# Performance work log

Hardware: AMD Instinct MI355X
Metric: run time of the kernel (lower is better)

Reference implementation:

```python
import jax, jax.numpy as jnp
import numpy as np

HEADS = 8


def setup_inputs() -> dict:
    key = jax.random.key(0)
    ks = jax.random.split(key, 7)
    B, C, H, W = 8, 512, 64, 64
    K, MEM = 64, 512
    s = 0.02
    return {
        "x": jax.random.normal(ks[0], (B, C, H, W), dtype=jnp.float32),
        "Ft": jax.random.normal(ks[1], (B, K, MEM), dtype=jnp.float32),
        "Wq": jax.random.normal(ks[2], (C, C), dtype=jnp.float32) * s,
        "Wk": jax.random.normal(ks[3], (C, MEM), dtype=jnp.float32) * s,
        "Wv": jax.random.normal(ks[4], (C, MEM), dtype=jnp.float32) * s,
        "Wp": jax.random.normal(ks[5], (C, C), dtype=jnp.float32) * s,
        "bp": jax.random.normal(ks[6], (C,), dtype=jnp.float32) * s,
    }


def reference(x, Ft, Wq, Wk, Wv, Wp, bp):
    B, C, H, W = x.shape
    h = HEADS
    d = C // h
    N = H * W
    # 1x1 conv query projection: (out_c, in_c) applied over spatial dims
    q = jnp.einsum('oc,bchw->bohw', Wq, x).reshape(B, h, d, N)
    q = jnp.transpose(q, (0, 1, 3, 2))                      # [B,h,N,d]
    # Linear K/V on memory tokens: Ft [B,K,MEM] @ W^T -> [B,K,C]
    k = (Ft @ Wk.T).reshape(B, -1, h, d).transpose(0, 2, 1, 3)  # [B,h,K,d]
    v = (Ft @ Wv.T).reshape(B, -1, h, d).transpose(0, 2, 1, 3)  # [B,h,K,d]
    attn = jnp.einsum('bhnc,bhkc->bhnk', q, k) / jnp.sqrt(jnp.float32(d))
    attn = jax.nn.softmax(attn, axis=-1)
    out = jnp.einsum('bhnk,bhkc->bhnc', attn, v)            # [B,h,N,d]
    out = jnp.transpose(out, (0, 1, 3, 2)).reshape(B, C, H, W)
    out = jnp.einsum('oc,bchw->bohw', Wp, out) + bp[None, :, None, None]
    return x + out
```

## Files before the change

### kernel.cpp

```cpp
#include <hip/hip_runtime.h>
#include <cstdint>
#include <cstddef>

#define BATCH 8
#define CDIM  512
#define NPIX  4096
#define NHEAD 8
#define DH    64
#define KTOK  64
#define MEM   512

#define SSTR 40
#define QSTR 72

typedef __attribute__((ext_vector_type(8))) short          bf8;
typedef __attribute__((ext_vector_type(4))) float          f4;
typedef __attribute__((ext_vector_type(4))) unsigned short us4;

__device__ __forceinline__ unsigned short f2bf(float f){
  union { float f; unsigned int u; } x; x.f = f;
  unsigned int r = (x.u + 0x7fffu + ((x.u >> 16) & 1u)) >> 16;
  return (unsigned short)r;
}

__global__ __launch_bounds__(256) void wconv(const float* __restrict__ wq, const float* __restrict__ wp,
                                             unsigned short* __restrict__ wqb, unsigned short* __restrict__ wpb){
  int i = (blockIdx.x * 256 + threadIdx.x) * 4;
  float4 a = *(const float4*)(wq + i);
  us4 pa = { f2bf(a.x), f2bf(a.y), f2bf(a.z), f2bf(a.w) };
  *(us4*)(wqb + i) = pa;
  float4 b = *(const float4*)(wp + i);
  us4 pb = { f2bf(b.x), f2bf(b.y), f2bf(b.z), f2bf(b.w) };
  *(us4*)(wpb + i) = pb;
}

__global__ __launch_bounds__(256) void xtrans(const float* __restrict__ x, unsigned short* __restrict__ xb){
  __shared__ __align__(16) unsigned short t[64 * 68];
  int tid = threadIdx.x;
  int n0 = blockIdx.x * 64, c0 = blockIdx.y * 64, b = blockIdx.z;
  const float* xp = x + ((size_t)(b * CDIM + c0)) * NPIX + n0;
#pragma unroll
  for (int it = 0; it < 4; ++it){
    int idx = it * 1024 + tid * 4;
    int cc = idx >> 6, nn = idx & 63;
    float4 v = *(const float4*)(xp + (size_t)cc * NPIX + nn);
    us4 pk = { f2bf(v.x), f2bf(v.y), f2bf(v.z), f2bf(v.w) };
    *(us4*)&t[cc * 68 + nn] = pk;
  }
  __syncthreads();
  unsigned short* op = xb + ((size_t)(b * NPIX + n0)) * CDIM + c0;
#pragma unroll
  for (int it = 0; it < 4; ++it){
    int idx = it * 1024 + tid * 4;
    int nn = idx >> 6, c4 = idx & 63;
    us4 pk = { t[(c4 + 0) * 68 + nn], t[(c4 + 1) * 68 + nn],
               t[(c4 + 2) * 68 + nn], t[(c4 + 3) * 68 + nn] };
    *(us4*)(op + (size_t)nn * CDIM + c4) = pk;
  }
}

__global__ __launch_bounds__(256) void kvproj(const float* __restrict__ Ft, const float* __restrict__ Wk,
                                              const float* __restrict__ Wv, unsigned short* __restrict__ kb,
                                              unsigned short* __restrict__ vt){
  __shared__ float ft[8][MEM];
  int tid = threadIdx.x;
  int cg = blockIdx.x, kk0 = blockIdx.y * 8, b = blockIdx.z;
  const float* fp = Ft + ((size_t)(b * KTOK + kk0)) * MEM;
#pragma unroll
  for (int it = 0; it < 4; ++it){
    int idx = it * 1024 + tid * 4;
    int row = idx >> 9, m = idx & 511;
    *(float4*)&ft[row][m] = *(const float4*)(fp + (size_t)row * MEM + m);
  }
  __syncthreads();
  int kv = tid >> 7, cl = tid & 127;
  int c = cg * 128 + cl;
  const float* wrow = (kv ? Wv : Wk) + (size_t)c * MEM;
  float acc[8] = {0.f,0.f,0.f,0.f,0.f,0.f,0.f,0.f};
  for (int m = 0; m < MEM; m += 4){
    float4 wv4 = *(const float4*)(wrow + m);
#pragma unroll
    for (int kk = 0; kk < 8; ++kk){
      acc[kk] += wv4.x * ft[kk][m] + wv4.y * ft[kk][m+1] + wv4.z * ft[kk][m+2] + wv4.w * ft[kk][m+3];
    }
  }
  int h = c >> 6, dd = c & 63;
  if (kv == 0){
#pragma unroll
    for (int kk = 0; kk < 8; ++kk)
      kb[(((size_t)(b * NHEAD + h)) * KTOK + kk0 + kk) * DH + dd] = f2bf(acc[kk] * 0.125f);
  } else {
#pragma unroll
    for (int kk = 0; kk < 8; ++kk)
      vt[(((size_t)(b * NHEAD + h)) * DH + dd) * KTOK + kk0 + kk] = f2bf(acc[kk]);
  }
}

__global__ __launch_bounds__(256, 2) void qattn(const unsigned short* __restrict__ wqb,
                                                const unsigned short* __restrict__ xb,
                                                const unsigned short* __restrict__ kb,
                                                const unsigned short* __restrict__ vt,
                                                unsigned short* __restrict__ att){
  __shared__ __align__(16) unsigned short ab[4 * 64 * QSTR];
  __shared__ __align__(16) unsigned short pbuf[4 * 64 * QSTR];
  int tid = threadIdx.x;
  int w = tid >> 6, l = tid & 63;
  int lo = l & 15, hi = l >> 4;
  int n0 = blockIdx.x * 128, o0 = blockIdx.y * 128, b = blockIdx.z;
  int ol = (w >> 1) * 64, nl = (w & 1) * 64;

  f4 z = {0.f, 0.f, 0.f, 0.f};
  f4 accq[4][4];
#pragma unroll
  for (int i = 0; i < 4; ++i)
#pragma unroll
    for (int j = 0; j < 4; ++j) accq[i][j] = z;

  int srow = tid >> 2;
  int scol = (tid & 3) * 8;
  const unsigned short* ap = wqb + ((size_t)(o0 + srow)) * CDIM + scol;
  const unsigned short* bp = xb + ((size_t)(b * NPIX + n0 + srow)) * CDIM + scol;
  unsigned short* as0 = &ab[srow * SSTR + scol];
  unsigned short* as1 = &ab[(srow + 64) * SSTR + scol];
  unsigned short* bs0 = &ab[5120 + srow * SSTR + scol];
  unsigned short* bs1 = &ab[5120 + (srow + 64) * SSTR + scol];

  for (int kc = 0; kc < CDIM; kc += 32){
    *(uint4*)as0 = *(const uint4*)(ap + kc);
    *(uint4*)as1 = *(const uint4*)(ap + 64 * CDIM + kc);
    *(uint4*)bs0 = *(const uint4*)(bp + kc);
    *(uint4*)bs1 = *(const uint4*)(bp + 64 * CDIM + kc);
    __syncthreads();
    bf8 af[4], bfr[4];
#pragma unroll
    for (int fi = 0; fi < 4; ++fi)
      af[fi] = *(const bf8*)&ab[(ol + fi * 16 + lo) * SSTR + hi * 8];
#pragma unroll
    for (int fj = 0; fj < 4; ++fj)
      bfr[fj] = *(const bf8*)&ab[5120 + (nl + fj * 16 + lo) * SSTR + hi * 8];
#pragma unroll
    for (int fi = 0; fi < 4; ++fi)
#pragma unroll
      for (int fj = 0; fj < 4; ++fj)
        accq[fi][fj] = __builtin_amdgcn_mfma_f32_16x16x32_bf16(af[fi], bfr[fj], accq[fi][fj], 0, 0, 0);
    __syncthreads();
  }

  unsigned short* qt = &ab[w * 64 * QSTR];
#pragma unroll
  for (int fi = 0; fi < 4; ++fi)
#pragma unroll
    for (int fj = 0; fj < 4; ++fj){
      f4 v = accq[fi][fj];
      us4 pk = { f2bf(v[0]), f2bf(v[1]), f2bf(v[2]), f2bf(v[3]) };
      *(us4*)&qt[(fj * 16 + lo) * QSTR + fi * 16 + hi * 4] = pk;
    }

  int head = blockIdx.y * 2 + (w >> 1);
  const unsigned short* kh = kb + ((size_t)(b * NHEAD + head)) * (KTOK * DH);
  f4 accs[4][4];
#pragma unroll
  for (int i = 0; i < 4; ++i)
#pragma unroll
    for (int j = 0; j < 4; ++j) accs[i][j] = z;
#pragma unroll
  for (int ks = 0; ks < 2; ++ks){
    bf8 ka[4];
#pragma unroll
    for (int fi = 0; fi < 4; ++fi)
      ka[fi] = *(const bf8*)(kh + (fi * 16 + lo) * 64 + ks * 32 + hi * 8);
#pragma unroll
    for (int fj = 0; fj < 4; ++fj){
      bf8 qf = *(const bf8*)&qt[(fj * 16 + lo) * QSTR + ks * 32 + hi * 8];
#pragma unroll
      for (int fi = 0; fi < 4; ++fi)
        accs[fi][fj] = __builtin_amdgcn_mfma_f32_16x16x32_bf16(ka[fi], qf, accs[fi][fj], 0, 0, 0);
    }
  }

#pragma unroll
  for (int fj = 0; fj < 4; ++fj){
    float mx = accs[0][fj][0];
#pragma unroll
    for (int fi = 0; fi < 4; ++fi)
#pragma unroll
      for (int r = 0; r < 4; ++r) mx = fmaxf(mx, accs[fi][fj][r]);
    mx = fmaxf(mx, __shfl_xor(mx, 16));
    mx = fmaxf(mx, __shfl_xor(mx, 32));
    float sm = 0.f;
#pragma unroll
    for (int fi = 0; fi < 4; ++fi)
#pragma unroll
      for (int r = 0; r < 4; ++r){
        float e = __expf(accs[fi][fj][r] - mx);
        accs[fi][fj][r] = e; sm += e;
      }
    sm += __shfl_xor(sm, 16);
    sm += __shfl_xor(sm, 32);
    float inv = 1.0f / sm;
#pragma unroll
    for (int fi = 0; fi < 4; ++fi){
      us4 pk = { f2bf(accs[fi][fj][0] * inv), f2bf(accs[fi][fj][1] * inv),
                 f2bf(accs[fi][fj][2] * inv), f2bf(accs[fi][fj][3] * inv) };
      *(us4*)&pbuf[w * 64 * QSTR + (fj * 16 + lo) * QSTR + fi * 16 + hi * 4] = pk;
    }
  }

  const unsigned short* vh = vt + ((size_t)(b * NHEAD + head)) * (DH * KTOK);
  f4 acco[4][4];
#pragma unroll
  for (int i = 0; i < 4; ++i)
#pragma unroll
    for (int j = 0; j < 4; ++j) acco[i][j] = z;
#pragma unroll
  for (int ks = 0; ks < 2; ++ks){
    bf8 va[4];
#pragma unroll
    for (int fi = 0; fi < 4; ++fi)
      va[fi] = *(const bf8*)(vh + (fi * 16 + lo) * 64 + ks * 32 + hi * 8);
#pragma unroll
    for (int fj = 0; fj < 4; ++fj){
      bf8 pf = *(const bf8*)&pbuf[w * 64 * QSTR + (fj * 16 + lo) * QSTR + ks * 32 + hi * 8];
#pragma unroll
      for (int fi = 0; fi < 4; ++fi)
        acco[fi][fj] = __builtin_amdgcn_mfma_f32_16x16x32_bf16(va[fi], pf, acco[fi][fj], 0, 0, 0);
    }
  }

  unsigned short* op = att + ((size_t)(b * NPIX + n0 + nl)) * CDIM + head * 64;
#pragma unroll
  for (int fi = 0; fi < 4; ++fi)
#pragma unroll
    for (int fj = 0; fj < 4; ++fj){
      f4 v = acco[fi][fj];
      us4 pk = { f2bf(v[0]), f2bf(v[1]), f2bf(v[2]), f2bf(v[3]) };
      *(us4*)(op + (size_t)(fj * 16 + lo) * CDIM + fi * 16 + hi * 4) = pk;
    }
}

__global__ __launch_bounds__(256, 2) void pproj(const unsigned short* __restrict__ wpb,
                                                const unsigned short* __restrict__ att,
                                                const float* __restrict__ x,
                                                const float* __restrict__ bpv,
                                                float* __restrict__ out){
  __shared__ __align__(16) unsigned short ab[2 * 128 * SSTR];
  int tid = threadIdx.x;
  int w = tid >> 6, l = tid & 63;
  int lo = l & 15, hi = l >> 4;
  int n0 = blockIdx.x * 128, o0 = blockIdx.y * 128, b = blockIdx.z;
  int ol = (w >> 1) * 64, nl = (w & 1) * 64;

  f4 z = {0.f, 0.f, 0.f, 0.f};
  f4 acc[4][4];
#pragma unroll
  for (int i = 0; i < 4; ++i)
#pragma unroll
    for (int j = 0; j < 4; ++j) acc[i][j] = z;

  int srow = tid >> 2;
  int scol = (tid & 3) * 8;
  const unsigned short* ap = wpb + ((size_t)(o0 + srow)) * CDIM + scol;
  const unsigned short* bp = att + ((size_t)(b * NPIX + n0 + srow)) * CDIM + scol;
  unsigned short* as0 = &ab[srow * SSTR + scol];
  unsigned short* as1 = &ab[(srow + 64) * SSTR + scol];
  unsigned short* bs0 = &ab[5120 + srow * SSTR + scol];
  unsigned short* bs1 = &ab[5120 + (srow + 64) * SSTR + scol];

  for (int kc = 0; kc < CDIM; kc += 32){
    *(uint4*)as0 = *(const uint4*)(ap + kc);
    *(uint4*)as1 = *(const uint4*)(ap + 64 * CDIM + kc);
    *(uint4*)bs0 = *(const uint4*)(bp + kc);
    *(uint4*)bs1 = *(const uint4*)(bp + 64 * CDIM + kc);
    __syncthreads();
    bf8 af[4], bfr[4];
#pragma unroll
    for (int fi = 0; fi < 4; ++fi)
      af[fi] = *(const bf8*)&ab[(ol + fi * 16 + lo) * SSTR + hi * 8];
#pragma unroll
    for (int fj = 0; fj < 4; ++fj)
      bfr[fj] = *(const bf8*)&ab[5120 + (nl + fj * 16 + lo) * SSTR + hi * 8];
#pragma unroll
    for (int fi = 0; fi < 4; ++fi)
#pragma unroll
      for (int fj = 0; fj < 4; ++fj)
        acc[fi][fj] = __builtin_amdgcn_mfma_f32_16x16x32_bf16(af[fi], bfr[fj], acc[fi][fj], 0, 0, 0);
    __syncthreads();
  }

#pragma unroll
  for (int fi = 0; fi < 4; ++fi)
#pragma unroll
    for (int fj = 0; fj < 4; ++fj){
      int o = o0 + ol + fi * 16 + hi * 4;
      int n = n0 + nl + fj * 16 + lo;
#pragma unroll
      for (int r = 0; r < 4; ++r){
        size_t idx = ((size_t)(b * CDIM + o + r)) * NPIX + n;
        out[idx] = acc[fi][fj][r] + bpv[o + r] + x[idx];
      }
    }
}

extern "C" void kernel_launch(void* const* d_in, const int* in_sizes, int n_in,
                              void* d_out, int out_size, void* d_ws, size_t ws_size,
                              hipStream_t stream){
  const float* x  = (const float*)d_in[0];
  const float* Ft = (const float*)d_in[1];
  const float* Wq = (const float*)d_in[2];
  const float* Wk = (const float*)d_in[3];
  const float* Wv = (const float*)d_in[4];
  const float* Wp = (const float*)d_in[5];
  const float* bp = (const float*)d_in[6];
  float* out = (float*)d_out;

  char* ws = (char*)d_ws;
  unsigned short* wqb = (unsigned short*)(ws);
  unsigned short* wpb = (unsigned short*)(ws + 524288);
  unsigned short* xb  = (unsigned short*)(ws + 1048576);
  unsigned short* att = (unsigned short*)(ws + 1048576 + 33554432);
  unsigned short* kb  = (unsigned short*)(ws + 1048576 + 2ull * 33554432);
  unsigned short* vt  = (unsigned short*)(ws + 1048576 + 2ull * 33554432 + 524288);

  wconv<<<dim3(256), dim3(256), 0, stream>>>(Wq, Wp, wqb, wpb);
  xtrans<<<dim3(64, 8, 8), dim3(256), 0, stream>>>(x, xb);
  kvproj<<<dim3(4, 8, 8), dim3(256), 0, stream>>>(Ft, Wk, Wv, kb, vt);
  qattn<<<dim3(32, 4, 8), dim3(256), 0, stream>>>(wqb, xb, kb, vt, att);
  pproj<<<dim3(32, 4, 8), dim3(256), 0, stream>>>(wpb, att, x, bp, out);
}
```

Before: 126.8 us.

## Register-prefetch K tiles with BK=64 and reuse LDS for P in GEMMs

Both GEMM main loops now use a K-tile of 64 instead of 32. Each loop prefetches the next tile into registers while MFMAs run on the current LDS tile, which halves the loop iterations and barriers and hides global load latency. In qattn the separate softmax probability buffer is dropped and P is written over the per-wave Q tile, keeping LDS at 36 KB. Launch bounds are raised to 4 blocks per CU, which may cause register spills given the prefetch registers plus 16 accumulator fragments.

New measurement: 261.7 us. +106.4%, slower.

```diff
diff --git a/kernel.cpp b/kernel.cpp
--- a/kernel.cpp
+++ b/kernel.cpp
@@ -10,8 +10,8 @@
 #define KTOK  64
 #define MEM   512
 
-#define SSTR 40
-#define QSTR 72
+#define BK    64
+#define TSTR  72
 
 typedef __attribute__((ext_vector_type(8))) short          bf8;
 typedef __attribute__((ext_vector_type(4))) float          f4;
@@ -96,13 +96,12 @@
   }
 }
 
-__global__ __launch_bounds__(256, 2) void qattn(const unsigned short* __restrict__ wqb,
+__global__ __launch_bounds__(256, 4) void qattn(const unsigned short* __restrict__ wqb,
                                                 const unsigned short* __restrict__ xb,
                                                 const unsigned short* __restrict__ kb,
                                                 const unsigned short* __restrict__ vt,
                                                 unsigned short* __restrict__ att){
-  __shared__ __align__(16) unsigned short ab[4 * 64 * QSTR];
-  __shared__ __align__(16) unsigned short pbuf[4 * 64 * QSTR];
+  __shared__ __align__(16) unsigned short ab[18432];
   int tid = threadIdx.x;
   int w = tid >> 6, l = tid & 63;
   int lo = l & 15, hi = l >> 4;
@@ -116,44 +115,62 @@
 #pragma unroll
     for (int j = 0; j < 4; ++j) accq[i][j] = z;
 
-  int srow = tid >> 2;
-  int scol = (tid & 3) * 8;
-  const unsigned short* ap = wqb + ((size_t)(o0 + srow)) * CDIM + scol;
-  const unsigned short* bp = xb + ((size_t)(b * NPIX + n0 + srow)) * CDIM + scol;
-  unsigned short* as0 = &ab[srow * SSTR + scol];
-  unsigned short* as1 = &ab[(srow + 64) * SSTR + scol];
-  unsigned short* bs0 = &ab[5120 + srow * SSTR + scol];
-  unsigned short* bs1 = &ab[5120 + (srow + 64) * SSTR + scol];
-
-  for (int kc = 0; kc < CDIM; kc += 32){
-    *(uint4*)as0 = *(const uint4*)(ap + kc);
-    *(uint4*)as1 = *(const uint4*)(ap + 64 * CDIM + kc);
-    *(uint4*)bs0 = *(const uint4*)(bp + kc);
-    *(uint4*)bs1 = *(const uint4*)(bp + 64 * CDIM + kc);
+  const int sr = tid >> 3;
+  const int sc = (tid & 7) * 8;
+  const unsigned short* ap = wqb + ((size_t)(o0 + sr)) * CDIM + sc;
+  const unsigned short* bp = xb + ((size_t)(b * NPIX + n0 + sr)) * CDIM + sc;
+  unsigned short* as = &ab[sr * TSTR + sc];
+  unsigned short* bs = &ab[9216 + sr * TSTR + sc];
+
+  uint4 ra[4], rb[4];
+#pragma unroll
+  for (int i = 0; i < 4; ++i){
+    ra[i] = *(const uint4*)(ap + (size_t)i * 32 * CDIM);
+    rb[i] = *(const uint4*)(bp + (size_t)i * 32 * CDIM);
+  }
+
+  for (int t = 0; t < 8; ++t){
     __syncthreads();
-    bf8 af[4], bfr[4];
-#pragma unroll
-    for (int fi = 0; fi < 4; ++fi)
-      af[fi] = *(const bf8*)&ab[(ol + fi * 16 + lo) * SSTR + hi * 8];
-#pragma unroll
-    for (int fj = 0; fj < 4; ++fj)
-      bfr[fj] = *(const bf8*)&ab[5120 + (nl + fj * 16 + lo) * SSTR + hi * 8];
-#pragma unroll
-    for (int fi = 0; fi < 4; ++fi)
+#pragma unroll
+    for (int i = 0; i < 4; ++i){
+      *(uint4*)(as + i * 32 * TSTR) = ra[i];
+      *(uint4*)(bs + i * 32 * TSTR) = rb[i];
+    }
+    __syncthreads();
+    if (t < 7){
+      int kc = (t + 1) * BK;
+#pragma unroll
+      for (int i = 0; i < 4; ++i){
+        ra[i] = *(const uint4*)(ap + (size_t)i * 32 * CDIM + kc);
+        rb[i] = *(const uint4*)(bp + (size_t)i * 32 * CDIM + kc);
+      }
+    }
+#pragma unroll
+    for (int ks = 0; ks < 2; ++ks){
+      bf8 af[4], bfr[4];
+#pragma unroll
+      for (int fi = 0; fi < 4; ++fi)
+        af[fi] = *(const bf8*)&ab[(ol + fi * 16 + lo) * TSTR + ks * 32 + hi * 8];
 #pragma unroll
       for (int fj = 0; fj < 4; ++fj)
-        accq[fi][fj] = __builtin_amdgcn_mfma_f32_16x16x32_bf16(af[fi], bfr[fj], accq[fi][fj], 0, 0, 0);
-    __syncthreads();
-  }
-
-  unsigned short* qt = &ab[w * 64 * QSTR];
+        bfr[fj] = *(const bf8*)&ab[9216 + (nl + fj * 16 + lo) * TSTR + ks * 32 + hi * 8];
+#pragma unroll
+      for (int fi = 0; fi < 4; ++fi)
+#pragma unroll
+        for (int fj = 0; fj < 4; ++fj)
+          accq[fi][fj] = __builtin_amdgcn_mfma_f32_16x16x32_bf16(af[fi], bfr[fj], accq[fi][fj], 0, 0, 0);
+    }
+  }
+  __syncthreads();
+
+  unsigned short* qt = &ab[w * 4608];
 #pragma unroll
   for (int fi = 0; fi < 4; ++fi)
 #pragma unroll
     for (int fj = 0; fj < 4; ++fj){
       f4 v = accq[fi][fj];
       us4 pk = { f2bf(v[0]), f2bf(v[1]), f2bf(v[2]), f2bf(v[3]) };
-      *(us4*)&qt[(fj * 16 + lo) * QSTR + fi * 16 + hi * 4] = pk;
+      *(us4*)&qt[(fj * 16 + lo) * TSTR + fi * 16 + hi * 4] = pk;
     }
 
   int head = blockIdx.y * 2 + (w >> 1);
@@ -171,7 +188,7 @@
       ka[fi] = *(const bf8*)(kh + (fi * 16 + lo) * 64 + ks * 32 + hi * 8);
 #pragma unroll
     for (int fj = 0; fj < 4; ++fj){
-      bf8 qf = *(const bf8*)&qt[(fj * 16 + lo) * QSTR + ks * 32 + hi * 8];
+      bf8 qf = *(const bf8*)&qt[(fj * 16 + lo) * TSTR + ks * 32 + hi * 8];
 #pragma unroll
       for (int fi = 0; fi < 4; ++fi)
         accs[fi][fj] = __builtin_amdgcn_mfma_f32_16x16x32_bf16(ka[fi], qf, accs[fi][fj], 0, 0, 0);
@@ -202,7 +219,7 @@
     for (int fi = 0; fi < 4; ++fi){
       us4 pk = { f2bf(accs[fi][fj][0] * inv), f2bf(accs[fi][fj][1] * inv),
                  f2bf(accs[fi][fj][2] * inv), f2bf(accs[fi][fj][3] * inv) };
-      *(us4*)&pbuf[w * 64 * QSTR + (fj * 16 + lo) * QSTR + fi * 16 + hi * 4] = pk;
+      *(us4*)&qt[(fj * 16 + lo) * TSTR + fi * 16 + hi * 4] = pk;
     }
   }
 
@@ -220,7 +237,7 @@
       va[fi] = *(const bf8*)(vh + (fi * 16 + lo) * 64 + ks * 32 + hi * 8);
 #pragma unroll
     for (int fj = 0; fj < 4; ++fj){
-      bf8 pf = *(const bf8*)&pbuf[w * 64 * QSTR + (fj * 16 + lo) * QSTR + ks * 32 + hi * 8];
+      bf8 pf = *(const bf8*)&qt[(fj * 16 + lo) * TSTR + ks * 32 + hi * 8];
 #pragma unroll
       for (int fi = 0; fi < 4; ++fi)
         acco[fi][fj] = __builtin_amdgcn_mfma_f32_16x16x32_bf16(va[fi], pf, acco[fi][fj], 0, 0, 0);
@@ -238,12 +255,12 @@
     }
 }
 
-__global__ __launch_bounds__(256, 2) void pproj(const unsigned short* __restrict__ wpb,
+__global__ __launch_bounds__(256, 4) void pproj(const unsigned short* __restrict__ wpb,
                                                 const unsigned short* __restrict__ att,
                                                 const float* __restrict__ x,
                                                 const float* __restrict__ bpv,
                                                 float* __restrict__ out){
-  __shared__ __align__(16) unsigned short ab[2 * 128 * SSTR];
+  __shared__ __align__(16) unsigned short ab[18432];
   int tid = threadIdx.x;
   int w = tid >> 6, l = tid & 63;
   int lo = l & 15, hi = l >> 4;
@@ -257,34 +274,51 @@
 #pragma unroll
     for (int j = 0; j < 4; ++j) acc[i][j] = z;
 
-  int srow = tid >> 2;
-  int scol = (tid & 3) * 8;
-  const unsigned short* ap = wpb + ((size_t)(o0 + srow)) * CDIM + scol;
-  const unsigned short* bp = att + ((size_t)(b * NPIX + n0 + srow)) * CDIM + scol;
-  unsigned short* as0 = &ab[srow * SSTR + scol];
-  unsigned short* as1 = &ab[(srow + 64) * SSTR + scol];
-  unsigned short* bs0 = &ab[5120 + srow * SSTR + scol];
-  unsigned short* bs1 = &ab[5120 + (srow + 64) * SSTR + scol];
-
-  for (int kc = 0; kc < CDIM; kc += 32){
-    *(uint4*)as0 = *(const uint4*)(ap + kc);
-    *(uint4*)as1 = *(const uint4*)(ap + 64 * CDIM + kc);
-    *(uint4*)bs0 = *(const uint4*)(bp + kc);
-    *(uint4*)bs1 = *(const uint4*)(bp + 64 * CDIM + kc);
+  const int sr = tid >> 3;
+  const int sc = (tid & 7) * 8;
+  const unsigned short* ap = wpb + ((size_t)(o0 + sr)) * CDIM + sc;
+  const unsigned short* bp = att + ((size_t)(b * NPIX + n0 + sr)) * CDIM + sc;
+  unsigned short* as = &ab[sr * TSTR + sc];
+  unsigned short* bs = &ab[9216 + sr * TSTR + sc];
+
+  uint4 ra[4], rb[4];
+#pragma unroll
+  for (int i = 0; i < 4; ++i){
+    ra[i] = *(const uint4*)(ap + (size_t)i * 32 * CDIM);
+    rb[i] = *(const uint4*)(bp + (size_t)i * 32 * CDIM);
+  }
+
+  for (int t = 0; t < 8; ++t){
     __syncthreads();
-    bf8 af[4], bfr[4];
-#pragma unroll
-    for (int fi = 0; fi < 4; ++fi)
-      af[fi] = *(const bf8*)&ab[(ol + fi * 16 + lo) * SSTR + hi * 8];
-#pragma unroll
-    for (int fj = 0; fj < 4; ++fj)
-      bfr[fj] = *(const bf8*)&ab[5120 + (nl + fj * 16 + lo) * SSTR + hi * 8];
-#pragma unroll
-    for (int fi = 0; fi < 4; ++fi)
+#pragma unroll
+    for (int i = 0; i < 4; ++i){
+      *(uint4*)(as + i * 32 * TSTR) = ra[i];
+      *(uint4*)(bs + i * 32 * TSTR) = rb[i];
+    }
+    __syncthreads();
+    if (t < 7){
+      int kc = (t + 1) * BK;
+#pragma unroll
+      for (int i = 0; i < 4; ++i){
+        ra[i] = *(const uint4*)(ap + (size_t)i * 32 * CDIM + kc);
+        rb[i] = *(const uint4*)(bp + (size_t)i * 32 * CDIM + kc);
+      }
+    }
+#pragma unroll
+    for (int ks = 0; ks < 2; ++ks){
+      bf8 af[4], bfr[4];
+#pragma unroll
+      for (int fi = 0; fi < 4; ++fi)
+        af[fi] = *(const bf8*)&ab[(ol + fi * 16 + lo) * TSTR + ks * 32 + hi * 8];
 #pragma unroll
       for (int fj = 0; fj < 4; ++fj)
-        acc[fi][fj] = __builtin_amdgcn_mfma_f32_16x16x32_bf16(af[fi], bfr[fj], acc[fi][fj], 0, 0, 0);
-    __syncthreads();
+        bfr[fj] = *(const bf8*)&ab[9216 + (nl + fj * 16 + lo) * TSTR + ks * 32 + hi * 8];
+#pragma unroll
+      for (int fi = 0; fi < 4; ++fi)
+#pragma unroll
+        for (int fj = 0; fj < 4; ++fj)
+          acc[fi][fj] = __builtin_amdgcn_mfma_f32_16x16x32_bf16(af[fi], bfr[fj], acc[fi][fj], 0, 0, 0);
+    }
   }
 
 #pragma unroll
```

## Use direct global-to-LDS loads with XOR-swizzled BK=64 tiles in GEMM kernels

Applied to the files above, without the earlier changes.

Both the Q-projection/attention kernel and the output projection kernel now stage A/B tiles with global_load_lds (direct global-to-LDS DMA) instead of going through registers. The K-chunk grows from 32 to 64, and the padded LDS strides are replaced by an XOR swizzle to avoid bank conflicts. The separate P buffer is merged into the Q tile buffer, which cuts LDS use and allows three blocks per CU in the launch bounds. The intent is to remove register-staging overhead and halve the number of barriers. The cost is a more intricate swizzled addressing scheme and no double buffering, so loads and compute still serialize on each barrier.

After: 115.7 us. 8.7% less time.

```diff
diff --git a/kernel.cpp b/kernel.cpp
--- a/kernel.cpp
+++ b/kernel.cpp
@@ -10,8 +10,7 @@
 #define KTOK  64
 #define MEM   512
 
-#define SSTR 40
-#define QSTR 72
+#define BK    64
 
 typedef __attribute__((ext_vector_type(8))) short          bf8;
 typedef __attribute__((ext_vector_type(4))) float          f4;
@@ -21,6 +20,11 @@
   union { float f; unsigned int u; } x; x.f = f;
   unsigned int r = (x.u + 0x7fffu + ((x.u >> 16) & 1u)) >> 16;
   return (unsigned short)r;
+}
+
+__device__ __forceinline__ void gld_lds16(const unsigned short* g, unsigned short* lds){
+  __builtin_amdgcn_global_load_lds((const __attribute__((address_space(1))) unsigned int*)g,
+                                   (__attribute__((address_space(3))) unsigned int*)lds, 16, 0, 0);
 }
 
 __global__ __launch_bounds__(256) void wconv(const float* __restrict__ wq, const float* __restrict__ wp,
@@ -96,13 +100,12 @@
   }
 }
 
-__global__ __launch_bounds__(256, 2) void qattn(const unsigned short* __restrict__ wqb,
+__global__ __launch_bounds__(256, 3) void qattn(const unsigned short* __restrict__ wqb,
                                                 const unsigned short* __restrict__ xb,
                                                 const unsigned short* __restrict__ kb,
                                                 const unsigned short* __restrict__ vt,
                                                 unsigned short* __restrict__ att){
-  __shared__ __align__(16) unsigned short ab[4 * 64 * QSTR];
-  __shared__ __align__(16) unsigned short pbuf[4 * 64 * QSTR];
+  __shared__ __align__(16) unsigned short ab[16384];
   int tid = threadIdx.x;
   int w = tid >> 6, l = tid & 63;
   int lo = l & 15, hi = l >> 4;
@@ -116,44 +119,51 @@
 #pragma unroll
     for (int j = 0; j < 4; ++j) accq[i][j] = z;
 
-  int srow = tid >> 2;
-  int scol = (tid & 3) * 8;
-  const unsigned short* ap = wqb + ((size_t)(o0 + srow)) * CDIM + scol;
-  const unsigned short* bp = xb + ((size_t)(b * NPIX + n0 + srow)) * CDIM + scol;
-  unsigned short* as0 = &ab[srow * SSTR + scol];
-  unsigned short* as1 = &ab[(srow + 64) * SSTR + scol];
-  unsigned short* bs0 = &ab[5120 + srow * SSTR + scol];
-  unsigned short* bs1 = &ab[5120 + (srow + 64) * SSTR + scol];
-
-  for (int kc = 0; kc < CDIM; kc += 32){
-    *(uint4*)as0 = *(const uint4*)(ap + kc);
-    *(uint4*)as1 = *(const uint4*)(ap + 64 * CDIM + kc);
-    *(uint4*)bs0 = *(const uint4*)(bp + kc);
-    *(uint4*)bs1 = *(const uint4*)(bp + 64 * CDIM + kc);
+  const int lrow = l >> 3;
+  const int lcc  = (l & 7) ^ lrow;
+  const unsigned short* asrc = wqb + ((size_t)(o0 + w * 8 + lrow)) * CDIM + lcc * 8;
+  const unsigned short* bsrc = xb + ((size_t)(b * NPIX + n0 + w * 8 + lrow)) * CDIM + lcc * 8;
+
+  for (int t = 0; t < 8; ++t){
+    int kc = t * BK;
+#pragma unroll
+    for (int j = 0; j < 4; ++j){
+      int g = j * 4 + w;
+      gld_lds16(asrc + (size_t)j * 32 * CDIM + kc, &ab[g * 512]);
+      gld_lds16(bsrc + (size_t)j * 32 * CDIM + kc, &ab[8192 + g * 512]);
+    }
     __syncthreads();
-    bf8 af[4], bfr[4];
-#pragma unroll
-    for (int fi = 0; fi < 4; ++fi)
-      af[fi] = *(const bf8*)&ab[(ol + fi * 16 + lo) * SSTR + hi * 8];
-#pragma unroll
-    for (int fj = 0; fj < 4; ++fj)
-      bfr[fj] = *(const bf8*)&ab[5120 + (nl + fj * 16 + lo) * SSTR + hi * 8];
-#pragma unroll
-    for (int fi = 0; fi < 4; ++fi)
+#pragma unroll
+    for (int ks = 0; ks < 2; ++ks){
+      int cc = ks * 4 + hi;
+      int sw = ((cc ^ (lo & 7)) << 3);
+      bf8 af[4], bfr[4];
+#pragma unroll
+      for (int fi = 0; fi < 4; ++fi)
+        af[fi] = *(const bf8*)&ab[(ol + fi * 16 + lo) * 64 + sw];
 #pragma unroll
       for (int fj = 0; fj < 4; ++fj)
-        accq[fi][fj] = __builtin_amdgcn_mfma_f32_16x16x32_bf16(af[fi], bfr[fj], accq[fi][fj], 0, 0, 0);
+        bfr[fj] = *(const bf8*)&ab[8192 + (nl + fj * 16 + lo) * 64 + sw];
+#pragma unroll
+      for (int fi = 0; fi < 4; ++fi)
+#pragma unroll
+        for (int fj = 0; fj < 4; ++fj)
+          accq[fi][fj] = __builtin_amdgcn_mfma_f32_16x16x32_bf16(af[fi], bfr[fj], accq[fi][fj], 0, 0, 0);
+    }
     __syncthreads();
   }
 
-  unsigned short* qt = &ab[w * 64 * QSTR];
+  unsigned short* qt = &ab[w * 4096];
 #pragma unroll
   for (int fi = 0; fi < 4; ++fi)
 #pragma unroll
     for (int fj = 0; fj < 4; ++fj){
       f4 v = accq[fi][fj];
       us4 pk = { f2bf(v[0]), f2bf(v[1]), f2bf(v[2]), f2bf(v[3]) };
-      *(us4*)&qt[(fj * 16 + lo) * QSTR + fi * 16 + hi * 4] = pk;
+      int row = fj * 16 + lo;
+      int col = fi * 16 + hi * 4;
+      int cs  = (((col >> 3) ^ (row & 7)) << 3) | (col & 7);
+      *(us4*)&qt[row * 64 + cs] = pk;
     }
 
   int head = blockIdx.y * 2 + (w >> 1);
@@ -165,13 +175,14 @@
     for (int j = 0; j < 4; ++j) accs[i][j] = z;
 #pragma unroll
   for (int ks = 0; ks < 2; ++ks){
+    int sw = (((ks * 4 + hi) ^ (lo & 7)) << 3);
     bf8 ka[4];
 #pragma unroll
     for (int fi = 0; fi < 4; ++fi)
       ka[fi] = *(const bf8*)(kh + (fi * 16 + lo) * 64 + ks * 32 + hi * 8);
 #pragma unroll
     for (int fj = 0; fj < 4; ++fj){
-      bf8 qf = *(const bf8*)&qt[(fj * 16 + lo) * QSTR + ks * 32 + hi * 8];
+      bf8 qf = *(const bf8*)&qt[(fj * 16 + lo) * 64 + sw];
 #pragma unroll
       for (int fi = 0; fi < 4; ++fi)
         accs[fi][fj] = __builtin_amdgcn_mfma_f32_16x16x32_bf16(ka[fi], qf, accs[fi][fj], 0, 0, 0);
@@ -202,7 +213,10 @@
     for (int fi = 0; fi < 4; ++fi){
       us4 pk = { f2bf(accs[fi][fj][0] * inv), f2bf(accs[fi][fj][1] * inv),
                  f2bf(accs[fi][fj][2] * inv), f2bf(accs[fi][fj][3] * inv) };
-      *(us4*)&pbuf[w * 64 * QSTR + (fj * 16 + lo) * QSTR + fi * 16 + hi * 4] = pk;
+      int row = fj * 16 + lo;
+      int col = fi * 16 + hi * 4;
+      int cs  = (((col >> 3) ^ (row & 7)) << 3) | (col & 7);
+      *(us4*)&qt[row * 64 + cs] = pk;
     }
   }
 
@@ -214,13 +228,14 @@
     for (int j = 0; j < 4; ++j) acco[i][j] = z;
 #pragma unroll
   for (int ks = 0; ks < 2; ++ks){
+    int sw = (((ks * 4 + hi) ^ (lo & 7)) << 3);
     bf8 va[4];
 #pragma unroll
     for (int fi = 0; fi < 4; ++fi)
       va[fi] = *(const bf8*)(vh + (fi * 16 + lo) * 64 + ks * 32 + hi * 8);
 #pragma unroll
     for (int fj = 0; fj < 4; ++fj){
-      bf8 pf = *(const bf8*)&pbuf[w * 64 * QSTR + (fj * 16 + lo) * QSTR + ks * 32 + hi * 8];
+      bf8 pf = *(const bf8*)&qt[(fj * 16 + lo) * 64 + sw];
 #pragma unroll
       for (int fi = 0; fi < 4; ++fi)
         acco[fi][fj] = __builtin_amdgcn_mfma_f32_16x16x32_bf16(va[fi], pf, acco[fi][fj], 0, 0, 0);
@@ -238,12 +253,12 @@
     }
 }
 
-__global__ __launch_bounds__(256, 2) void pproj(const unsigned short* __restrict__ wpb,
+__global__ __launch_bounds__(256, 3) void pproj(const unsigned short* __restrict__ wpb,
                                                 const unsigned short* __restrict__ att,
                                                 const float* __restrict__ x,
                                                 const float* __restrict__ bpv,
                                                 float* __restrict__ out){
-  __shared__ __align__(16) unsigned short ab[2 * 128 * SSTR];
+  __shared__ __align__(16) unsigned short ab[16384];
   int tid = threadIdx.x;
   int w = tid >> 6, l = tid & 63;
   int lo = l & 15, hi = l >> 4;
@@ -257,33 +272,37 @@
 #pragma unroll
     for (int j = 0; j < 4; ++j) acc[i][j] = z;
 
-  int srow = tid >> 2;
-  int scol = (tid & 3) * 8;
-  const unsigned short* ap = wpb + ((size_t)(o0 + srow)) * CDIM + scol;
-  const unsigned short* bp = att + ((size_t)(b * NPIX + n0 + srow)) * CDIM + scol;
-  unsigned short* as0 = &ab[srow * SSTR + scol];
-  unsigned short* as1 = &ab[(srow + 64) * SSTR + scol];
-  unsigned short* bs0 = &ab[5120 + srow * SSTR + scol];
-  unsigned short* bs1 = &ab[5120 + (srow + 64) * SSTR + scol];
-
-  for (int kc = 0; kc < CDIM; kc += 32){
-    *(uint4*)as0 = *(const uint4*)(ap + kc);
-    *(uint4*)as1 = *(const uint4*)(ap + 64 * CDIM + kc);
-    *(uint4*)bs0 = *(const uint4*)(bp + kc);
-    *(uint4*)bs1 = *(const uint4*)(bp + 64 * CDIM + kc);
+  const int lrow = l >> 3;
+  const int lcc  = (l & 7) ^ lrow;
+  const unsigned short* asrc = wpb + ((size_t)(o0 + w * 8 + lrow)) * CDIM + lcc * 8;
+  const unsigned short* bsrc = att + ((size_t)(b * NPIX + n0 + w * 8 + lrow)) * CDIM + lcc * 8;
+
+  for (int t = 0; t < 8; ++t){
+    int kc = t * BK;
+#pragma unroll
+    for (int j = 0; j < 4; ++j){
+      int g = j * 4 + w;
+      gld_lds16(asrc + (size_t)j * 32 * CDIM + kc, &ab[g * 512]);
+      gld_lds16(bsrc + (size_t)j * 32 * CDIM + kc, &ab[8192 + g * 512]);
+    }
     __syncthreads();
-    bf8 af[4], bfr[4];
-#pragma unroll
-    for (int fi = 0; fi < 4; ++fi)
-      af[fi] = *(const bf8*)&ab[(ol + fi * 16 + lo) * SSTR + hi * 8];
-#pragma unroll
-    for (int fj = 0; fj < 4; ++fj)
-      bfr[fj] = *(const bf8*)&ab[5120 + (nl + fj * 16 + lo) * SSTR + hi * 8];
-#pragma unroll
-    for (int fi = 0; fi < 4; ++fi)
+#pragma unroll
+    for (int ks = 0; ks < 2; ++ks){
+      int cc = ks * 4 + hi;
+      int sw = ((cc ^ (lo & 7)) << 3);
+      bf8 af[4], bfr[4];
+#pragma unroll
+      for (int fi = 0; fi < 4; ++fi)
+        af[fi] = *(const bf8*)&ab[(ol + fi * 16 + lo) * 64 + sw];
 #pragma unroll
       for (int fj = 0; fj < 4; ++fj)
-        acc[fi][fj] = __builtin_amdgcn_mfma_f32_16x16x32_bf16(af[fi], bfr[fj], acc[fi][fj], 0, 0, 0);
+        bfr[fj] = *(const bf8*)&ab[8192 + (nl + fj * 16 + lo) * 64 + sw];
+#pragma unroll
+      for (int fi = 0; fi < 4; ++fi)
+#pragma unroll
+        for (int fj = 0; fj < 4; ++fj)
+          acc[fi][fj] = __builtin_amdgcn_mfma_f32_16x16x32_bf16(af[fi], bfr[fj], acc[fi][fj], 0, 0, 0);
+    }
     __syncthreads();
   }
 
```
